# Kernel tuning notes

Hardware: AMD Instinct MI355X
Metric: run time of the kernel (lower is better)

The kernel has to match this reference:

```python
import jax, jax.numpy as jnp
import numpy as np

V_MAX = 3.0
FEATURE_CLAMP = 10.0
TOP_K = 1


def _green_diag(d):
    """Diagonal of G = (tridiag(sub=1, diag=d, super=1))^{-1} for each batch row.
    d: (B, N) complex64. Stable two-sided continued-fraction (Thomas-like) recurrences:
      L_i = d_i - 1/L_{i-1},  U_i = d_i - 1/U_{i+1},  G_ii = 1/(L_i + U_i - d_i).
    Sequential over N (vectorized over B) via lax.scan.
    """
    dT = d.T  # (N, B)

    def step(c, di):
        nc = di - 1.0 / c
        return nc, nc

    L0 = dT[0]
    _, Lr = jax.lax.scan(step, L0, dT[1:])
    L = jnp.concatenate([L0[None], Lr], axis=0)  # (N, B)

    dR = dT[::-1]
    U0 = dR[0]
    _, Ur = jax.lax.scan(step, U0, dR[1:])
    U = jnp.concatenate([U0[None], Ur], axis=0)[::-1]  # (N, B)

    return (1.0 / (L + U - dT)).T  # (B, N)


def setup_inputs() -> dict:
    key = jax.random.key(0)
    B, N, D, E, F = 4, 4096, 512, 4, 2048
    ks = jax.random.split(key, 8)
    s = lambda k, sh, sc: (jax.random.normal(k, sh, jnp.float32) * sc)
    return dict(
        x=jax.random.normal(ks[0], (B, N, D), jnp.float32),
        v_proj_w=s(ks[1], (1, D), D ** -0.5),
        v_proj_b=jnp.zeros((1,), jnp.float32),
        gamma=jnp.float32(0.0),
        epsilon_param=jnp.float32(1.0),
        gate_w=s(ks[2], (E, D), D ** -0.5),
        gate_b=jnp.zeros((E,), jnp.float32),
        w1=s(ks[3], (E, D, F), D ** -0.5),
        b1=jnp.zeros((E, F), jnp.float32),
        w2=s(ks[4], (E, F, D), F ** -0.5),
        b2=jnp.zeros((E, D), jnp.float32),
        out_w=s(ks[5], (D, 2), 0.5),
        out_b=jnp.zeros((D,), jnp.float32),
        bk_scale=jnp.ones((D,), jnp.float32),
    )


def reference(x, v_proj_w, v_proj_b, gamma, epsilon_param, gate_w, gate_b,
              w1, b1, w2, b2, out_w, out_b, bk_scale):
    # 1) scalar potential from tokens
    v = jnp.einsum('bnd,od->bno', x, v_proj_w)[..., 0] + v_proj_b[0]  # (B, N)
    v = jnp.clip(v, -V_MAX, V_MAX)

    # 2) gamma-shifted complex tridiagonal Green's function diagonal
    eps = jax.nn.softplus(epsilon_param) + 1e-6
    z = 1j * (eps + gamma)                       # complex64 scalar
    d = ((v - 2.0).astype(jnp.complex64) - z)    # he_diag - z, (B, N)
    G = _green_diag(d)                            # (B, N) complex
    feats = jnp.clip(jnp.stack([G.real, G.imag], axis=-1), -FEATURE_CLAMP, FEATURE_CLAMP)  # (B,N,2)

    # 3) sparse MoE FFN (top-1 routing, experts = Linear -> GELU -> Linear)
    logits = jnp.einsum('bnd,ed->bne', x, gate_w) + gate_b
    probs = jax.nn.softmax(logits, axis=-1)
    top_p, top_i = jax.lax.top_k(probs, TOP_K)
    top_w = top_p / jnp.sum(top_p, axis=-1, keepdims=True)
    wmask = jnp.sum(jax.nn.one_hot(top_i, probs.shape[-1], dtype=probs.dtype) * top_w[..., None], axis=-2)  # (B,N,E)

    h = jax.nn.gelu(jnp.einsum('bnd,edf->benf', x, w1) + b1[None, :, None, :], approximate=False)
    y = jnp.einsum('benf,efd->bend', h, w2) + b2[None, :, None, :]
    ffn_out = jnp.einsum('bne,bend->bnd', wmask, y)

    # 4) combine spectral features with FFN output
    spec_out = jnp.einsum('bnc,dc->bnd', feats, out_w) + out_b
    return ffn_out + bk_scale * spec_out
```

## Files before the change

### kernel.cpp

```cpp
#include <hip/hip_runtime.h>
#include <hip/hip_bf16.h>
#include <math.h>


typedef __bf16 bf16x8 __attribute__((ext_vector_type(8)));
typedef float  f32x4  __attribute__((ext_vector_type(4)));
typedef __attribute__((address_space(3))) __bf16 lbf16;

#define B_   4
#define N_   4096
#define D_   512
#define E_   4
#define F_   2048
#define T_   (B_*N_)
#define CAP_ T_
#define R256 68
#define PADROWS (R256*256)

#define LGKM_BARRIER() asm volatile("s_waitcnt lgkmcnt(0)\n\ts_barrier" ::: "memory")

__device__ __forceinline__ void gload_lds16(const __bf16* g, lbf16* l) {
    __builtin_amdgcn_global_load_lds(
        (__attribute__((address_space(1))) void*)(void*)g,
        (__attribute__((address_space(3))) void*)l, 16, 0, 0);
}

__device__ __forceinline__ float fast_gelu(float x) {
    float u = 1.5957691216f * fmaf(0.044715f * x, x * x, x);
    return x / (1.0f + __expf(-u));
}

__device__ __forceinline__ void load8f2(const float2* p, float2* dst) {
    const float4* q = (const float4*)p;
    #pragma unroll
    for (int i = 0; i < 4; ++i) {
        float4 t = q[i];
        dst[2*i]   = make_float2(t.x, t.y);
        dst[2*i+1] = make_float2(t.z, t.w);
    }
}

__device__ __forceinline__ void mfma_tile(const char* Ab, const char* Bb,
                                          int cs0, int cs1, f32x4 acc[4][4]) {
    #pragma unroll
    for (int ks = 0; ks < 2; ++ks) {
        int cs = ks ? cs1 : cs0;
        bf16x8 af[4], bfr[4];
        #pragma unroll
        for (int m = 0; m < 4; ++m)
            af[m] = *(const bf16x8*)(Ab + m * 2048 + cs);
        #pragma unroll
        for (int n = 0; n < 4; ++n)
            bfr[n] = *(const bf16x8*)(Bb + n * 2048 + cs);
        #pragma unroll
        for (int m = 0; m < 4; ++m)
            #pragma unroll
            for (int n = 0; n < 4; ++n)
                acc[m][n] = __builtin_amdgcn_mfma_f32_16x16x32_bf16(af[m], bfr[n], acc[m][n], 0, 0, 0);
    }
}

__device__ alignas(256) __bf16 s_w1t[(size_t)E_*F_*D_];
__device__ alignas(256) __bf16 s_w2t[(size_t)E_*D_*F_];
__device__ alignas(256) __bf16 s_xb[(size_t)PADROWS*D_];
__device__ alignas(256) __bf16 s_H[(size_t)PADROWS*F_];
__device__ alignas(256) float2 s_d[T_];
__device__ alignas(256) float2 s_feats[T_];
__device__ alignas(256) float2 s_L[T_];
__device__ alignas(256) float2 s_U[T_];
__device__ alignas(256) int    s_perm[E_*CAP_];
__device__ alignas(256) int    s_cnt[E_];
__device__ alignas(256) int    s_tpre[8];
__device__ alignas(256) int    s_eid[T_];

__device__ inline float dot8(float4 a, float4 b, float4 c, float4 d) {
    float s =      a.x * c.x;
    s = fmaf(a.y, c.y, s); s = fmaf(a.z, c.z, s); s = fmaf(a.w, c.w, s);
    s = fmaf(b.x, d.x, s); s = fmaf(b.y, d.y, s); s = fmaf(b.z, d.z, s);
    s = fmaf(b.w, d.w, s);
    return s;
}

__device__ inline float wave_sum(float s) {
    #pragma unroll
    for (int off = 32; off > 0; off >>= 1) s += __shfl_xor(s, off);
    return s;
}

__global__ __launch_bounds__(256) void prep_trans_kernel(
        const float* __restrict__ w1, const float* __restrict__ w2,
        __bf16* __restrict__ w1t, __bf16* __restrict__ w2t,
        const float* __restrict__ x,
        const float* __restrict__ vw, const float* __restrict__ vb,
        const float* __restrict__ gamma, const float* __restrict__ epsp,
        const float* __restrict__ gw, const float* __restrict__ gb,
        float2* __restrict__ dbuf, int* __restrict__ eid) {
    __shared__ alignas(16) float tile[32][33];
    int idx = blockIdx.x;
    int tid = threadIdx.x;
    if (idx < 8192) {
        int which = idx >> 12;
        int r = idx & 4095;
        int e = r >> 10;
        int t = r & 1023;
        int R, C, c0, r0;
        const float* s;
        __bf16* d;
        if (which == 0) { R = D_; C = F_; c0 = (t & 63) * 32; r0 = (t >> 6) * 32;
                          s = w1 + (size_t)e * R * C; d = w1t + (size_t)e * R * C; }
        else            { R = F_; C = D_; c0 = (t & 15) * 32; r0 = (t >> 4) * 32;
                          s = w2 + (size_t)e * R * C; d = w2t + (size_t)e * R * C; }
        int tx = tid & 31, ty = tid >> 5;
        #pragma unroll
        for (int i = 0; i < 4; ++i)
            tile[ty + i*8][tx] = s[(size_t)(r0 + ty + i*8) * C + c0 + tx];
        __syncthreads();
        #pragma unroll
        for (int i = 0; i < 4; ++i)
            d[(size_t)(c0 + ty + i*8) * R + r0 + tx] = (__bf16)tile[tx][ty + i*8];
    } else {
        int wv = tid >> 6, lane = tid & 63;
        int token = (idx - 8192) * 4 + wv;
        const float4* xr = (const float4*)(x + (size_t)token * D_);
        float4 xa = xr[lane*2], xb = xr[lane*2 + 1];

        const float4* vr = (const float4*)vw;
        float sv = dot8(xa, xb, vr[lane*2], vr[lane*2 + 1]);
        float sg0, sg1, sg2, sg3;
        {
            const float4* g0 = (const float4*)(gw + 0*D_);
            const float4* g1 = (const float4*)(gw + 1*D_);
            const float4* g2 = (const float4*)(gw + 2*D_);
            const float4* g3 = (const float4*)(gw + 3*D_);
            sg0 = dot8(xa, xb, g0[lane*2], g0[lane*2+1]);
            sg1 = dot8(xa, xb, g1[lane*2], g1[lane*2+1]);
            sg2 = dot8(xa, xb, g2[lane*2], g2[lane*2+1]);
            sg3 = dot8(xa, xb, g3[lane*2], g3[lane*2+1]);
        }
        sv  = wave_sum(sv);
        sg0 = wave_sum(sg0); sg1 = wave_sum(sg1);
        sg2 = wave_sum(sg2); sg3 = wave_sum(sg3);

        if (lane == 0) {
            float v = sv + vb[0];
            v = fminf(fmaxf(v, -3.0f), 3.0f);
            float eps = log1pf(expf(epsp[0])) + 1e-6f;
            dbuf[token] = make_float2(v - 2.0f, -(eps + gamma[0]));

            float l0 = sg0 + gb[0], l1 = sg1 + gb[1], l2 = sg2 + gb[2], l3 = sg3 + gb[3];
            float best = l0; int be = 0;
            if (l1 > best) { best = l1; be = 1; }
            if (l2 > best) { best = l2; be = 2; }
            if (l3 > best) { best = l3; be = 3; }
            eid[token] = be;
        }
    }
}

__global__ __launch_bounds__(1024) void route_scan_kernel(
        const int* __restrict__ eid, int* __restrict__ perm,
        int* __restrict__ cnt, int* __restrict__ tpre,
        const float2* __restrict__ dbuf, float2* __restrict__ Lb,
        float2* __restrict__ Ub, float2* __restrict__ feats) {
    int tid = threadIdx.x;
    if (blockIdx.x == 0) {
        __shared__ int chunkcnt[256][4];
        __shared__ int chunkoff[256][4];
        __shared__ int totals[4];
        int wv = tid >> 6, lane = tid & 63;

        for (int c = wv; c < 256; c += 16) {
            int e = eid[c * 64 + lane];
            unsigned long long m0 = __ballot(e == 0);
            unsigned long long m1 = __ballot(e == 1);
            unsigned long long m2 = __ballot(e == 2);
            unsigned long long m3 = __ballot(e == 3);
            if (lane == 0) {
                chunkcnt[c][0] = __popcll(m0);
                chunkcnt[c][1] = __popcll(m1);
                chunkcnt[c][2] = __popcll(m2);
                chunkcnt[c][3] = __popcll(m3);
            }
        }
        __syncthreads();

        if (wv < 4) {
            int e = wv, carry = 0;
            #pragma unroll
            for (int g = 0; g < 4; ++g) {
                int idx = g * 64 + lane;
                int v = chunkcnt[idx][e];
                int s = v;
                #pragma unroll
                for (int off = 1; off < 64; off <<= 1) {
                    int u = __shfl_up(s, off);
                    if (lane >= off) s += u;
                }
                chunkoff[idx][e] = carry + s - v;
                carry += __shfl(s, 63);
            }
            if (lane == 0) { cnt[e] = carry; totals[e] = carry; }
        }
        __syncthreads();
        if (tid == 0) {
            int acc = 0;
            #pragma unroll
            for (int e = 0; e < E_; ++e) { tpre[e] = acc; acc += (totals[e] + 255) >> 8; }
            tpre[4] = acc;
        }

        for (int c = wv; c < 256; c += 16) {
            int t = c * 64 + lane;
            int e = eid[t];
            unsigned long long m0 = __ballot(e == 0);
            unsigned long long m1 = __ballot(e == 1);
            unsigned long long m2 = __ballot(e == 2);
            unsigned long long m3 = __ballot(e == 3);
            unsigned long long mym = (e == 0) ? m0 : (e == 1) ? m1 : (e == 2) ? m2 : m3;
            unsigned long long below = lane ? (mym & ((1ull << lane) - 1ull)) : 0ull;
            int pos = chunkoff[c][e] + __popcll(below);
            perm[e * CAP_ + pos] = t;
        }
    } else {
        __shared__ alignas(16) float chunkM[8][64][8];
        __shared__ alignas(16) float bound[8][64][4];
        int s = tid >> 6, c = tid & 63;
        int b = s & 3, dir = (s >> 2) & 1;

        if (tid < 512) {
            float ar=1, ai=0, br=0, bi=0, cr=0, ci=0, dr=1, di=0;
            float2 cur[8], nxt[8];
            {
                int seq0 = c * 64;
                const float2* p = dbuf + (dir ? (b*N_ + N_ - 8 - seq0) : (b*N_ + seq0));
                load8f2(p, cur);
            }
            for (int g = 0; g < 8; ++g) {
                if (g < 7) {
                    int seq0 = c * 64 + (g + 1) * 8;
                    const float2* p = dbuf + (dir ? (b*N_ + N_ - 8 - seq0) : (b*N_ + seq0));
                    load8f2(p, nxt);
                }
                #pragma unroll
                for (int q = 0; q < 8; ++q) {
                    float2 dv = dir ? cur[7 - q] : cur[q];
                    float nar = dv.x*ar - dv.y*ai - cr;
                    float nai = dv.x*ai + dv.y*ar - ci;
                    float nbr = dv.x*br - dv.y*bi - dr;
                    float nbi = dv.x*bi + dv.y*br - di;
                    cr = ar; ci = ai; dr = br; di = bi;
                    ar = nar; ai = nai; br = nbr; bi = nbi;
                }
                float m = fmaxf(fmaxf(fmaxf(fabsf(ar),fabsf(ai)),fmaxf(fabsf(br),fabsf(bi))),
                                fmaxf(fmaxf(fabsf(cr),fabsf(ci)),fmaxf(fabsf(dr),fabsf(di))));
                float inv = 1.0f / fmaxf(m, 1e-30f);
                ar*=inv; ai*=inv; br*=inv; bi*=inv; cr*=inv; ci*=inv; dr*=inv; di*=inv;
                #pragma unroll
                for (int q = 0; q < 8; ++q) cur[q] = nxt[q];
            }
            float* cm = chunkM[s][c];
            cm[0]=ar; cm[1]=ai; cm[2]=br; cm[3]=bi; cm[4]=cr; cm[5]=ci; cm[6]=dr; cm[7]=di;
        }
        __syncthreads();

        if (tid < 8) {
            int ss = tid;
            float pr=1, pi=0, qr=0, qi=0;
            for (int cc = 0; cc < 64; ++cc) {
                float* bd = bound[ss][cc];
                bd[0]=pr; bd[1]=pi; bd[2]=qr; bd[3]=qi;
                const float* m = chunkM[ss][cc];
                float npr = m[0]*pr - m[1]*pi + m[2]*qr - m[3]*qi;
                float npi = m[0]*pi + m[1]*pr + m[2]*qi + m[3]*qr;
                float nqr = m[4]*pr - m[5]*pi + m[6]*qr - m[7]*qi;
                float nqi = m[4]*pi + m[5]*pr + m[6]*qi + m[7]*qr;
                float mx = fmaxf(fmaxf(fabsf(npr),fabsf(npi)), fmaxf(fabsf(nqr),fabsf(nqi)));
                float inv = 1.0f / fmaxf(mx, 1e-30f);
                pr = npr*inv; pi = npi*inv; qr = nqr*inv; qi = nqi*inv;
            }
        }
        __syncthreads();

        if (tid < 512) {
            const float* bd = bound[s][c];
            float pr=bd[0], pi=bd[1], qr=bd[2], qi=bd[3];
            float den = fmaxf(pr*pr + pi*pi, 1e-30f);
            float invr = (qr*pr + qi*pi) / den;
            float invi = (qi*pr - qr*pi) / den;
            float2 cur[8], nxt[8];
            {
                int seq0 = c * 64;
                const float2* p = dbuf + (dir ? (b*N_ + N_ - 8 - seq0) : (b*N_ + seq0));
                load8f2(p, cur);
            }
            for (int g = 0; g < 8; ++g) {
                if (g < 7) {
                    int seq0 = c * 64 + (g + 1) * 8;
                    const float2* p = dbuf + (dir ? (b*N_ + N_ - 8 - seq0) : (b*N_ + seq0));
                    load8f2(p, nxt);
                }
                #pragma unroll
                for (int q = 0; q < 8; ++q) {
                    int seq = c * 64 + g * 8 + q;
                    int orig = dir ? (N_ - 1 - seq) : seq;
                    int t = b * N_ + orig;
                    float2 dv = dir ? cur[7 - q] : cur[q];
                    float Lr = dv.x - invr, Li = dv.y - invi;
                    if (dir) Ub[t] = make_float2(Lr, Li);
                    else     Lb[t] = make_float2(Lr, Li);
                    float d2 = Lr*Lr + Li*Li;
                    invr = Lr / d2; invi = -Li / d2;
                }
                #pragma unroll
                for (int q = 0; q < 8; ++q) cur[q] = nxt[q];
            }
        }
        __threadfence();
        __syncthreads();

        for (int t = tid; t < T_; t += 1024) {
            float2 L = Lb[t], U = Ub[t], dv = dbuf[t];
            float sr = L.x + U.x - dv.x;
            float si = L.y + U.y - dv.y;
            float den = sr*sr + si*si;
            float Gr = sr / den, Gi = -si / den;
            Gr = fminf(fmaxf(Gr, -10.0f), 10.0f);
            Gi = fminf(fmaxf(Gi, -10.0f), 10.0f);
            feats[t] = make_float2(Gr, Gi);
        }
    }
}

__global__ __launch_bounds__(256) void reorder_kernel(
        const float* __restrict__ x, const int* __restrict__ perm,
        const int* __restrict__ cnt, const int* __restrict__ tpre,
        __bf16* __restrict__ xb) {
    int wv = threadIdx.x >> 6, lane = threadIdx.x & 63;
    int prow = blockIdx.x * 4 + wv;
    if (prow >= tpre[4] * 256) return;
    int e = 0;
    #pragma unroll
    for (int k = 1; k < E_; ++k) if (prow >= tpre[k] * 256) e = k;
    int i = prow - tpre[e] * 256;
    int token = (i < cnt[e]) ? perm[e * CAP_ + i] : -1;
    bf16x8 v = {0,0,0,0,0,0,0,0};
    if (token >= 0) {
        const float4* xr = (const float4*)(x + (size_t)token * D_);
        float4 a = xr[lane*2], b = xr[lane*2 + 1];
        v = (bf16x8){(__bf16)a.x,(__bf16)a.y,(__bf16)a.z,(__bf16)a.w,
                     (__bf16)b.x,(__bf16)b.y,(__bf16)b.z,(__bf16)b.w};
    }
    *(bf16x8*)(xb + (size_t)prow * D_ + lane * 8) = v;
}

__global__ __launch_bounds__(512, 4) void gemm1_kernel(
        const __bf16* __restrict__ xb, const __bf16* __restrict__ w1t,
        const float* __restrict__ b1, __bf16* __restrict__ Hb,
        const int* __restrict__ tpre) {
    int bid = blockIdx.x;
    int lb  = (bid & 7) * 136 + (bid >> 3);
    int rt = lb >> 4, ct = lb & 15;
    if (rt >= tpre[4]) return;
    int e = 0;
    #pragma unroll
    for (int k = 1; k < E_; ++k) if (rt >= tpre[k]) e = k;

    __shared__ __bf16 A[256 * 64];
    __shared__ __bf16 Bm[128 * 64];

    int tid = threadIdx.x, lane = tid & 63, wv = tid >> 6;
    int fl = lane & 15, gl = lane >> 4;
    int wr = wv >> 1, wc = wv & 1;

    int r8    = lane >> 3;
    int scolb = ((lane & 7) * 16) ^ (r8 << 4);
    const __bf16* aS0 = xb  + (size_t)(rt * 256 + wv * 32 + r8) * 512 + (scolb >> 1);
    const __bf16* bS0 = w1t + (size_t)(e * F_ + ct * 128 + wv * 16 + r8) * 512 + (scolb >> 1);
    lbf16* aD0 = (lbf16*)A  + wv * 32 * 64;
    lbf16* bD0 = (lbf16*)Bm + wv * 16 * 64;

    int xorv = (fl & 7) << 4;
    int cs0 = (gl * 16) ^ xorv;
    int cs1 = (64 + gl * 16) ^ xorv;
    const char* Ab = (const char*)A  + (wr * 64 + fl) * 128;
    const char* Bb = (const char*)Bm + (wc * 64 + fl) * 128;

    f32x4 acc[4][4];
    #pragma unroll
    for (int m = 0; m < 4; ++m)
        #pragma unroll
        for (int n = 0; n < 4; ++n) acc[m][n] = (f32x4){0.f,0.f,0.f,0.f};

    #pragma unroll
    for (int i = 0; i < 4; ++i)
        gload_lds16(aS0 + (size_t)i * 8 * 512, aD0 + i * 512);
    #pragma unroll
    for (int i = 0; i < 2; ++i)
        gload_lds16(bS0 + (size_t)i * 8 * 512, bD0 + i * 512);

    for (int kt = 0; kt < 8; ++kt) {
        __syncthreads();
        mfma_tile(Ab, Bb, cs0, cs1, acc);
        if (kt + 1 < 8) {
            LGKM_BARRIER();
            #pragma unroll
            for (int i = 0; i < 4; ++i)
                gload_lds16(aS0 + (size_t)i * 8 * 512 + (kt + 1) * 64, aD0 + i * 512);
            #pragma unroll
            for (int i = 0; i < 2; ++i)
                gload_lds16(bS0 + (size_t)i * 8 * 512 + (kt + 1) * 64, bD0 + i * 512);
        }
    }

    int gre = rt * 256 + wr * 64;
    int gce = ct * 128 + wc * 64;
    float b1v[4];
    #pragma unroll
    for (int n = 0; n < 4; ++n) b1v[n] = b1[e * F_ + gce + n*16 + fl];
    #pragma unroll
    for (int m = 0; m < 4; ++m)
        #pragma unroll
        for (int r = 0; r < 4; ++r) {
            __bf16* hrow = Hb + (size_t)(gre + m*16 + gl*4 + r) * F_ + gce;
            #pragma unroll
            for (int n = 0; n < 4; ++n)
                hrow[n*16 + fl] = (__bf16)fast_gelu(acc[m][n][r] + b1v[n]);
        }
}

__global__ __launch_bounds__(512, 4) void gemm2_kernel(
        const __bf16* __restrict__ Hb, const __bf16* __restrict__ w2t,
        const float* __restrict__ b2, const float* __restrict__ outw,
        const float* __restrict__ outb, const float* __restrict__ bk,
        const float2* __restrict__ feats, const int* __restrict__ perm,
        const int* __restrict__ cnt_p, const int* __restrict__ tpre,
        float* __restrict__ out) {
    int bid = blockIdx.x;
    int lb  = (bid & 7) * 34 + (bid >> 3);
    int rt = lb >> 2, ct = lb & 3;
    if (rt >= tpre[4]) return;
    int e = 0;
    #pragma unroll
    for (int k = 1; k < E_; ++k) if (rt >= tpre[k]) e = k;

    __shared__ __bf16 A[256 * 64];
    __shared__ __bf16 Bm[128 * 64];

    int tid = threadIdx.x, lane = tid & 63, wv = tid >> 6;
    int fl = lane & 15, gl = lane >> 4;
    int wr = wv >> 1, wc = wv & 1;

    int r8    = lane >> 3;
    int scolb = ((lane & 7) * 16) ^ (r8 << 4);
    const __bf16* aS0 = Hb  + (size_t)(rt * 256 + wv * 32 + r8) * F_ + (scolb >> 1);
    const __bf16* bS0 = w2t + (size_t)(e * D_ + ct * 128 + wv * 16 + r8) * F_ + (scolb >> 1);
    lbf16* aD0 = (lbf16*)A  + wv * 32 * 64;
    lbf16* bD0 = (lbf16*)Bm + wv * 16 * 64;

    int xorv = (fl & 7) << 4;
    int cs0 = (gl * 16) ^ xorv;
    int cs1 = (64 + gl * 16) ^ xorv;
    const char* Ab = (const char*)A  + (wr * 64 + fl) * 128;
    const char* Bb = (const char*)Bm + (wc * 64 + fl) * 128;

    f32x4 acc[4][4];
    #pragma unroll
    for (int m = 0; m < 4; ++m)
        #pragma unroll
        for (int n = 0; n < 4; ++n) acc[m][n] = (f32x4){0.f,0.f,0.f,0.f};

    #pragma unroll
    for (int i = 0; i < 4; ++i)
        gload_lds16(aS0 + (size_t)i * 8 * F_, aD0 + i * 512);
    #pragma unroll
    for (int i = 0; i < 2; ++i)
        gload_lds16(bS0 + (size_t)i * 8 * F_, bD0 + i * 512);

    for (int kt = 0; kt < 32; ++kt) {
        __syncthreads();
        mfma_tile(Ab, Bb, cs0, cs1, acc);
        if (kt + 1 < 32) {
            LGKM_BARRIER();
            #pragma unroll
            for (int i = 0; i < 4; ++i)
                gload_lds16(aS0 + (size_t)i * 8 * F_ + (kt + 1) * 64, aD0 + i * 512);
            #pragma unroll
            for (int i = 0; i < 2; ++i)
                gload_lds16(bS0 + (size_t)i * 8 * F_ + (kt + 1) * 64, bD0 + i * 512);
        }
    }

    int cnt = cnt_p[e];
    int ibase = rt * 256 + wr * 64 - tpre[e] * 256;
    int gce = ct * 128 + wc * 64;
    float c_b2[4], c_o0[4], c_o1[4], c_ob[4], c_bk[4];
    #pragma unroll
    for (int n = 0; n < 4; ++n) {
        int dcol = gce + n*16 + fl;
        c_b2[n] = b2[e * D_ + dcol];
        c_o0[n] = outw[dcol * 2 + 0];
        c_o1[n] = outw[dcol * 2 + 1];
        c_ob[n] = outb[dcol];
        c_bk[n] = bk[dcol];
    }
    #pragma unroll
    for (int m = 0; m < 4; ++m)
        #pragma unroll
        for (int r = 0; r < 4; ++r) {
            int i = ibase + m*16 + gl*4 + r;
            if (i >= cnt) continue;
            int token = perm[e * CAP_ + i];
            float2 ft = feats[token];
            float* orow = out + (size_t)token * D_;
            #pragma unroll
            for (int n = 0; n < 4; ++n) {
                int dcol = gce + n*16 + fl;
                float spec = ft.x * c_o0[n] + ft.y * c_o1[n] + c_ob[n];
                orow[dcol] = acc[m][n][r] + c_b2[n] + c_bk[n] * spec;
            }
        }
}

extern "C" void kernel_launch(void* const* d_in, const int* in_sizes, int n_in,
                              void* d_out, int out_size, void* d_ws, size_t ws_size,
                              hipStream_t stream) {
    const float* x     = (const float*)d_in[0];
    const float* vpw   = (const float*)d_in[1];
    const float* vpb   = (const float*)d_in[2];
    const float* gamma = (const float*)d_in[3];
    const float* epsp  = (const float*)d_in[4];
    const float* gw    = (const float*)d_in[5];
    const float* gb    = (const float*)d_in[6];
    const float* w1    = (const float*)d_in[7];
    const float* b1    = (const float*)d_in[8];
    const float* w2    = (const float*)d_in[9];
    const float* b2    = (const float*)d_in[10];
    const float* ow    = (const float*)d_in[11];
    const float* ob    = (const float*)d_in[12];
    const float* bk    = (const float*)d_in[13];
    float* out = (float*)d_out;

    const size_t szW  = (size_t)E_ * F_ * D_ * sizeof(__bf16);
    const size_t szF2 = (size_t)T_ * sizeof(float2);
    const size_t szPm = (size_t)E_ * CAP_ * sizeof(int);
    const size_t szCt = 256;
    const size_t szXb = (size_t)PADROWS * D_ * sizeof(__bf16);
    const size_t szH  = (size_t)PADROWS * F_ * sizeof(__bf16);
    const size_t szEi = (size_t)T_ * sizeof(int);
    size_t need = 2*szW + 4*szF2 + szPm + 2*szCt + szXb + szH + szEi + 16*256;

    __bf16 *w1t, *w2t, *xbuf, *Hbuf; float2 *dbuf, *Lb, *Ub, *feats;
    int *perm, *cnt, *tpre, *eid;
    int use_ws = (d_ws != nullptr && ws_size >= need);
    if (use_ws) {
        size_t off = 0;
        auto carve = [&](size_t bytes) {
            void* p = (char*)d_ws + off;
            off += (bytes + 255) & ~(size_t)255;
            return p;
        };
        w1t   = (__bf16*)carve(szW);
        w2t   = (__bf16*)carve(szW);
        xbuf  = (__bf16*)carve(szXb);
        Hbuf  = (__bf16*)carve(szH);
        dbuf  = (float2*)carve(szF2);
        Lb    = (float2*)carve(szF2);
        Ub    = (float2*)carve(szF2);
        feats = (float2*)carve(szF2);
        perm  = (int*)   carve(szPm);
        cnt   = (int*)   carve(szCt);
        tpre  = (int*)   carve(szCt);
        eid   = (int*)   carve(szEi);
    } else {
        void* p;
        hipGetSymbolAddress(&p, HIP_SYMBOL(s_w1t));  w1t   = (__bf16*)p;
        hipGetSymbolAddress(&p, HIP_SYMBOL(s_w2t));  w2t   = (__bf16*)p;
        hipGetSymbolAddress(&p, HIP_SYMBOL(s_xb));   xbuf  = (__bf16*)p;
        hipGetSymbolAddress(&p, HIP_SYMBOL(s_H));    Hbuf  = (__bf16*)p;
        hipGetSymbolAddress(&p, HIP_SYMBOL(s_d));    dbuf  = (float2*)p;
        hipGetSymbolAddress(&p, HIP_SYMBOL(s_L));    Lb    = (float2*)p;
        hipGetSymbolAddress(&p, HIP_SYMBOL(s_U));    Ub    = (float2*)p;
        hipGetSymbolAddress(&p, HIP_SYMBOL(s_feats));feats = (float2*)p;
        hipGetSymbolAddress(&p, HIP_SYMBOL(s_perm)); perm  = (int*)p;
        hipGetSymbolAddress(&p, HIP_SYMBOL(s_cnt));  cnt   = (int*)p;
        hipGetSymbolAddress(&p, HIP_SYMBOL(s_tpre)); tpre  = (int*)p;
        hipGetSymbolAddress(&p, HIP_SYMBOL(s_eid));  eid   = (int*)p;
    }

    prep_trans_kernel<<<12288, 256, 0, stream>>>(w1, w2, w1t, w2t,
                                                 x, vpw, vpb, gamma, epsp, gw, gb,
                                                 dbuf, eid);
    route_scan_kernel<<<2, 1024, 0, stream>>>(eid, perm, cnt, tpre, dbuf, Lb, Ub, feats);
    reorder_kernel<<<PADROWS/4, 256, 0, stream>>>(x, perm, cnt, tpre, xbuf);
    gemm1_kernel<<<R256*16, 512, 0, stream>>>(xbuf, w1t, b1, Hbuf, tpre);
    gemm2_kernel<<<R256*4, 512, 0, stream>>>(Hbuf, w2t, b2, ow, ob, bk,
                                             feats, perm, cnt, tpre, out);
}
```

Baseline: 198.8 us.

## Fuse token gather into GEMM1 and drop separate reorder kernel

The bf16 conversion of x moves into the prep kernel, which writes a token-ordered bf16 copy. GEMM1 then gathers A rows through the expert permutation directly in its global-to-LDS loads, so the separate reorder kernel launch and its padded gathered buffer are gone. Padding rows now load token 0 instead of zeros. Those rows feed H rows that gemm2 is presumably expected to ignore. Gathered loads are less contiguous across rows than the previous linear layout.

```diff
diff --git a/kernel.cpp b/kernel.cpp
--- a/kernel.cpp
+++ b/kernel.cpp
@@ -62,7 +62,7 @@
 
 __device__ alignas(256) __bf16 s_w1t[(size_t)E_*F_*D_];
 __device__ alignas(256) __bf16 s_w2t[(size_t)E_*D_*F_];
-__device__ alignas(256) __bf16 s_xb[(size_t)PADROWS*D_];
+__device__ alignas(256) __bf16 s_xl[(size_t)T_*D_];
 __device__ alignas(256) __bf16 s_H[(size_t)PADROWS*F_];
 __device__ alignas(256) float2 s_d[T_];
 __device__ alignas(256) float2 s_feats[T_];
@@ -94,7 +94,8 @@
         const float* __restrict__ vw, const float* __restrict__ vb,
         const float* __restrict__ gamma, const float* __restrict__ epsp,
         const float* __restrict__ gw, const float* __restrict__ gb,
-        float2* __restrict__ dbuf, int* __restrict__ eid) {
+        float2* __restrict__ dbuf, int* __restrict__ eid,
+        __bf16* __restrict__ xlin) {
     __shared__ alignas(16) float tile[32][33];
     int idx = blockIdx.x;
     int tid = threadIdx.x;
@@ -123,6 +124,10 @@
         int token = (idx - 8192) * 4 + wv;
         const float4* xr = (const float4*)(x + (size_t)token * D_);
         float4 xa = xr[lane*2], xb = xr[lane*2 + 1];
+
+        bf16x8 xv = {(__bf16)xa.x,(__bf16)xa.y,(__bf16)xa.z,(__bf16)xa.w,
+                     (__bf16)xb.x,(__bf16)xb.y,(__bf16)xb.z,(__bf16)xb.w};
+        *(bf16x8*)(xlin + (size_t)token * D_ + lane * 8) = xv;
 
         const float4* vr = (const float4*)vw;
         float sv = dot8(xa, xb, vr[lane*2], vr[lane*2 + 1]);
@@ -331,32 +336,11 @@
     }
 }
 
-__global__ __launch_bounds__(256) void reorder_kernel(
-        const float* __restrict__ x, const int* __restrict__ perm,
-        const int* __restrict__ cnt, const int* __restrict__ tpre,
-        __bf16* __restrict__ xb) {
-    int wv = threadIdx.x >> 6, lane = threadIdx.x & 63;
-    int prow = blockIdx.x * 4 + wv;
-    if (prow >= tpre[4] * 256) return;
-    int e = 0;
-    #pragma unroll
-    for (int k = 1; k < E_; ++k) if (prow >= tpre[k] * 256) e = k;
-    int i = prow - tpre[e] * 256;
-    int token = (i < cnt[e]) ? perm[e * CAP_ + i] : -1;
-    bf16x8 v = {0,0,0,0,0,0,0,0};
-    if (token >= 0) {
-        const float4* xr = (const float4*)(x + (size_t)token * D_);
-        float4 a = xr[lane*2], b = xr[lane*2 + 1];
-        v = (bf16x8){(__bf16)a.x,(__bf16)a.y,(__bf16)a.z,(__bf16)a.w,
-                     (__bf16)b.x,(__bf16)b.y,(__bf16)b.z,(__bf16)b.w};
-    }
-    *(bf16x8*)(xb + (size_t)prow * D_ + lane * 8) = v;
-}
-
 __global__ __launch_bounds__(512, 4) void gemm1_kernel(
-        const __bf16* __restrict__ xb, const __bf16* __restrict__ w1t,
+        const __bf16* __restrict__ xlin, const __bf16* __restrict__ w1t,
         const float* __restrict__ b1, __bf16* __restrict__ Hb,
-        const int* __restrict__ tpre) {
+        const int* __restrict__ tpre, const int* __restrict__ cnt_p,
+        const int* __restrict__ perm) {
     int bid = blockIdx.x;
     int lb  = (bid & 7) * 136 + (bid >> 3);
     int rt = lb >> 4, ct = lb & 15;
@@ -364,6 +348,8 @@
     int e = 0;
     #pragma unroll
     for (int k = 1; k < E_; ++k) if (rt >= tpre[k]) e = k;
+    int cnt = cnt_p[e];
+    int base = tpre[e] * 256;
 
     __shared__ __bf16 A[256 * 64];
     __shared__ __bf16 Bm[128 * 64];
@@ -374,7 +360,14 @@
 
     int r8    = lane >> 3;
     int scolb = ((lane & 7) * 16) ^ (r8 << 4);
-    const __bf16* aS0 = xb  + (size_t)(rt * 256 + wv * 32 + r8) * 512 + (scolb >> 1);
+    const __bf16* aS[4];
+    #pragma unroll
+    for (int i = 0; i < 4; ++i) {
+        int gr = rt * 256 + wv * 32 + r8 + i * 8;
+        int il = gr - base;
+        int token = (il < cnt) ? perm[e * CAP_ + il] : 0;
+        aS[i] = xlin + (size_t)token * D_ + (scolb >> 1);
+    }
     const __bf16* bS0 = w1t + (size_t)(e * F_ + ct * 128 + wv * 16 + r8) * 512 + (scolb >> 1);
     lbf16* aD0 = (lbf16*)A  + wv * 32 * 64;
     lbf16* bD0 = (lbf16*)Bm + wv * 16 * 64;
@@ -393,7 +386,7 @@
 
     #pragma unroll
     for (int i = 0; i < 4; ++i)
-        gload_lds16(aS0 + (size_t)i * 8 * 512, aD0 + i * 512);
+        gload_lds16(aS[i], aD0 + i * 512);
     #pragma unroll
     for (int i = 0; i < 2; ++i)
         gload_lds16(bS0 + (size_t)i * 8 * 512, bD0 + i * 512);
@@ -405,7 +398,7 @@
             LGKM_BARRIER();
             #pragma unroll
             for (int i = 0; i < 4; ++i)
-                gload_lds16(aS0 + (size_t)i * 8 * 512 + (kt + 1) * 64, aD0 + i * 512);
+                gload_lds16(aS[i] + (kt + 1) * 64, aD0 + i * 512);
             #pragma unroll
             for (int i = 0; i < 2; ++i)
                 gload_lds16(bS0 + (size_t)i * 8 * 512 + (kt + 1) * 64, bD0 + i * 512);
@@ -544,12 +537,12 @@
     const size_t szF2 = (size_t)T_ * sizeof(float2);
     const size_t szPm = (size_t)E_ * CAP_ * sizeof(int);
     const size_t szCt = 256;
-    const size_t szXb = (size_t)PADROWS * D_ * sizeof(__bf16);
+    const size_t szXl = (size_t)T_ * D_ * sizeof(__bf16);
     const size_t szH  = (size_t)PADROWS * F_ * sizeof(__bf16);
     const size_t szEi = (size_t)T_ * sizeof(int);
-    size_t need = 2*szW + 4*szF2 + szPm + 2*szCt + szXb + szH + szEi + 16*256;
-
-    __bf16 *w1t, *w2t, *xbuf, *Hbuf; float2 *dbuf, *Lb, *Ub, *feats;
+    size_t need = 2*szW + 4*szF2 + szPm + 2*szCt + szXl + szH + szEi + 16*256;
+
+    __bf16 *w1t, *w2t, *xlin, *Hbuf; float2 *dbuf, *Lb, *Ub, *feats;
     int *perm, *cnt, *tpre, *eid;
     int use_ws = (d_ws != nullptr && ws_size >= need);
     if (use_ws) {
@@ -561,7 +554,7 @@
         };
         w1t   = (__bf16*)carve(szW);
         w2t   = (__bf16*)carve(szW);
-        xbuf  = (__bf16*)carve(szXb);
+        xlin  = (__bf16*)carve(szXl);
         Hbuf  = (__bf16*)carve(szH);
         dbuf  = (float2*)carve(szF2);
         Lb    = (float2*)carve(szF2);
@@ -575,7 +568,7 @@
         void* p;
         hipGetSymbolAddress(&p, HIP_SYMBOL(s_w1t));  w1t   = (__bf16*)p;
         hipGetSymbolAddress(&p, HIP_SYMBOL(s_w2t));  w2t   = (__bf16*)p;
-        hipGetSymbolAddress(&p, HIP_SYMBOL(s_xb));   xbuf  = (__bf16*)p;
+        hipGetSymbolAddress(&p, HIP_SYMBOL(s_xl));   xlin  = (__bf16*)p;
         hipGetSymbolAddress(&p, HIP_SYMBOL(s_H));    Hbuf  = (__bf16*)p;
         hipGetSymbolAddress(&p, HIP_SYMBOL(s_d));    dbuf  = (float2*)p;
         hipGetSymbolAddress(&p, HIP_SYMBOL(s_L));    Lb    = (float2*)p;
@@ -589,10 +582,9 @@
 
     prep_trans_kernel<<<12288, 256, 0, stream>>>(w1, w2, w1t, w2t,
                                                  x, vpw, vpb, gamma, epsp, gw, gb,
-                                                 dbuf, eid);
+                                                 dbuf, eid, xlin);
     route_scan_kernel<<<2, 1024, 0, stream>>>(eid, perm, cnt, tpre, dbuf, Lb, Ub, feats);
-    reorder_kernel<<<PADROWS/4, 256, 0, stream>>>(x, perm, cnt, tpre, xbuf);
-    gemm1_kernel<<<R256*16, 512, 0, stream>>>(xbuf, w1t, b1, Hbuf, tpre);
+    gemm1_kernel<<<R256*16, 512, 0, stream>>>(xlin, w1t, b1, Hbuf, tpre, cnt, perm);
     gemm2_kernel<<<R256*4, 512, 0, stream>>>(Hbuf, w2t, b2, ow, ob, bk,
                                              feats, perm, cnt, tpre, out);
 }
```

After: 194.7 us, median of 2. 1.02x faster.
